# Performance work log

Hardware: AMD Instinct MI355X
Metric: run time of the kernel (lower is better)

## Reference

```python
import jax, jax.numpy as jnp
import numpy as np

HS = 1024
IMS = 4096
NHEAD = 16
EPS = 1e-5


def _layer_norm(x, g, b):
    mu = jnp.mean(x, axis=-1, keepdims=True)
    var = jnp.mean(jnp.square(x - mu), axis=-1, keepdims=True)
    return (x - mu) * jax.lax.rsqrt(var + EPS) * g + b


def setup_inputs() -> dict:
    key = jax.random.key(0)
    ks = jax.random.split(key, 10)
    B, S = 16, 512
    x = jax.random.normal(ks[0], (B, S, HS), dtype=jnp.float32)
    input_mask = jnp.zeros((B, S), dtype=jnp.float32)  # additive mask, 0 = attend
    sc = 0.02
    return {
        "x": x,
        "input_mask": input_mask,
        "qkv_w": jax.random.normal(ks[1], (3 * HS, HS), jnp.float32) * sc,
        "qkv_b": jnp.zeros((3 * HS,), jnp.float32),
        "attn_ow": jax.random.normal(ks[2], (HS, HS), jnp.float32) * sc,
        "attn_ob": jnp.zeros((HS,), jnp.float32),
        "ln1_g": jnp.ones((HS,), jnp.float32),
        "ln1_b": jnp.zeros((HS,), jnp.float32),
        "inter_w": jax.random.normal(ks[3], (IMS, HS), jnp.float32) * sc,
        "inter_b": jnp.zeros((IMS,), jnp.float32),
        "out_w": jax.random.normal(ks[4], (HS, IMS), jnp.float32) * sc,
        "out_b": jnp.zeros((HS,), jnp.float32),
        "ln2_g": jnp.ones((HS,), jnp.float32),
        "ln2_b": jnp.zeros((HS,), jnp.float32),
    }


def reference(x, input_mask, qkv_w, qkv_b, attn_ow, attn_ob, ln1_g, ln1_b,
              inter_w, inter_b, out_w, out_b, ln2_g, ln2_b):
    B, S, H = x.shape
    d = H // NHEAD
    # ---- self-attention block (pre_layer_norm=True, eval mode => no dropout) ----
    resid = x
    y = _layer_norm(x, ln1_g, ln1_b)
    qkv = jnp.einsum('bsh,eh->bse', y, qkv_w) + qkv_b  # [B,S,3H]
    q, k, v = jnp.split(qkv, 3, axis=-1)
    q = q.reshape(B, S, NHEAD, d)
    k = k.reshape(B, S, NHEAD, d)
    v = v.reshape(B, S, NHEAD, d)
    scores = jnp.einsum('bqnd,bknd->bnqk', q, k) / jnp.sqrt(jnp.float32(d))
    scores = scores + input_mask[:, None, None, :]  # additive padding mask
    probs = jax.nn.softmax(scores, axis=-1)
    ctx = jnp.einsum('bnqk,bknd->bqnd', probs, v).reshape(B, S, H)
    attn_out = jnp.einsum('bsh,oh->bso', ctx, attn_ow) + attn_ob
    x = resid + attn_out
    # ---- FFN block ----
    resid = x
    y = _layer_norm(x, ln2_g, ln2_b)
    h = jax.nn.relu(jnp.einsum('bsh,ih->bsi', y, inter_w) + inter_b)
    ffn_out = jnp.einsum('bsi,oi->bso', h, out_w) + out_b
    return resid + ffn_out
```

## Files before the change

kernel.cpp:

```cpp
#include <hip/hip_runtime.h>


using f32x4  = __attribute__((ext_vector_type(4))) float;
using f32x16 = __attribute__((ext_vector_type(16))) float;
using s16x8  = __attribute__((ext_vector_type(8))) short;
using i32x4  = __attribute__((ext_vector_type(4))) int;

__device__ __forceinline__ unsigned short f2bf(float f) {
    unsigned x = __builtin_bit_cast(unsigned, f);
    return (unsigned short)((x + 0x7fffu + ((x >> 16) & 1u)) >> 16);
}

#define GLL16(gptr, lptr)                                                     \
    __builtin_amdgcn_global_load_lds(                                         \
        (const __attribute__((address_space(1))) void*)(gptr),                \
        (__attribute__((address_space(3))) void*)(lptr), 16, 0, 0)

__global__ __launch_bounds__(256) void wconv_kernel(
    const float* __restrict__ w0, const float* __restrict__ w1,
    const float* __restrict__ w2, const float* __restrict__ w3,
    unsigned short* __restrict__ o0, unsigned short* __restrict__ o1,
    unsigned short* __restrict__ o2, unsigned short* __restrict__ o3) {
    long idx = (long)blockIdx.x * 256 + threadIdx.x;
    const float* src;
    unsigned short* dst;
    long rel;
    if (idx < 786432L)        { src = w0; dst = o0; rel = idx; }
    else if (idx < 1048576L)  { src = w1; dst = o1; rel = idx - 786432L; }
    else if (idx < 2097152L)  { src = w2; dst = o2; rel = idx - 1048576L; }
    else                      { src = w3; dst = o3; rel = idx - 2097152L; }
    float4 v = *(const float4*)(src + rel * 4);
    ushort4 o;
    o.x = f2bf(v.x); o.y = f2bf(v.y); o.z = f2bf(v.z); o.w = f2bf(v.w);
    *(ushort4*)(dst + rel * 4) = o;
}

__global__ __launch_bounds__(256) void ln_kernel(
    const float* __restrict__ x, const float* __restrict__ gw,
    const float* __restrict__ bw, unsigned short* __restrict__ y) {
    __shared__ float rbuf[8];
    const int row = blockIdx.x;
    const int t = threadIdx.x;
    const float* xr = x + (size_t)row * 1024;
    float4 v = *(const float4*)(xr + t * 4);
    float s  = v.x + v.y + v.z + v.w;
    float ss = v.x * v.x + v.y * v.y + v.z * v.z + v.w * v.w;
#pragma unroll
    for (int sh = 1; sh < 64; sh <<= 1) {
        s  += __shfl_xor(s, sh, 64);
        ss += __shfl_xor(ss, sh, 64);
    }
    int w = t >> 6;
    if ((t & 63) == 0) { rbuf[w * 2] = s; rbuf[w * 2 + 1] = ss; }
    __syncthreads();
    s  = rbuf[0] + rbuf[2] + rbuf[4] + rbuf[6];
    ss = rbuf[1] + rbuf[3] + rbuf[5] + rbuf[7];
    float mu  = s * (1.f / 1024.f);
    float var = ss * (1.f / 1024.f) - mu * mu;
    float rs  = rsqrtf(var + 1e-5f);
    float4 gv = *(const float4*)(gw + t * 4);
    float4 bv = *(const float4*)(bw + t * 4);
    ushort4 o;
    o.x = f2bf((v.x - mu) * rs * gv.x + bv.x);
    o.y = f2bf((v.y - mu) * rs * gv.y + bv.y);
    o.z = f2bf((v.z - mu) * rs * gv.z + bv.z);
    o.w = f2bf((v.w - mu) * rs * gv.w + bv.w);
    *(ushort4*)(y + (size_t)row * 1024 + t * 4) = o;
}

template <bool RELU, bool RESID, bool OUT_BF16>
__global__ __launch_bounds__(256, 2) void gemm_bt(
    const unsigned short* __restrict__ A, const unsigned short* __restrict__ Bw,
    const float* __restrict__ bias, const float* __restrict__ resid,
    void* __restrict__ Cout, int M, int N, int K) {
    __shared__ char smem[2 * 128 * 64 * 2];
    char* As = smem;
    char* Bs = smem + 128 * 64 * 2;

    const int tid = threadIdx.x;
    const int lane = tid & 63;
    const int w = tid >> 6;
    const int wr = w >> 1, wc = w & 1;
    const int g = lane >> 4;
    const int fr = lane & 15;
    const int nwg = gridDim.x * gridDim.y;
    const int L = blockIdx.y * gridDim.x + blockIdx.x;
    const int swz = (L & 7) * (nwg >> 3) + (L >> 3);
    const int m0 = (swz / gridDim.x) * 128;
    const int n0 = (swz % gridDim.x) * 128;

    f32x4 acc[4][4] = {};

    for (int kt = 0; kt < K; kt += 64) {
#pragma unroll
        for (int c = 0; c < 4; ++c) {
            int lin = (c * 256 + tid) * 16;
            int row = lin >> 7;
            int Lb = lin ^ ((row & 7) << 4);
            int colb = Lb & 127;
            const char* ga = (const char*)A + ((size_t)(m0 + row) * K + kt) * 2 + colb;
            const char* gb = (const char*)Bw + ((size_t)(n0 + row) * K + kt) * 2 + colb;
            GLL16(ga, As + lin);
            GLL16(gb, Bs + lin);
        }
        __syncthreads();
#pragma unroll
        for (int ks = 0; ks < 2; ++ks) {
            s16x8 af[4], bf[4];
#pragma unroll
            for (int mi = 0; mi < 4; ++mi) {
                int row = wr * 64 + mi * 16 + fr;
                int off = (row << 7) + ((ks * 64 + g * 16) ^ ((row & 7) << 4));
                af[mi] = *(const s16x8*)(As + off);
            }
#pragma unroll
            for (int ni = 0; ni < 4; ++ni) {
                int row = wc * 64 + ni * 16 + fr;
                int off = (row << 7) + ((ks * 64 + g * 16) ^ ((row & 7) << 4));
                bf[ni] = *(const s16x8*)(Bs + off);
            }
#pragma unroll
            for (int mi = 0; mi < 4; ++mi)
#pragma unroll
                for (int ni = 0; ni < 4; ++ni)
                    acc[mi][ni] = __builtin_amdgcn_mfma_f32_16x16x32_bf16(
                        af[mi], bf[ni], acc[mi][ni], 0, 0, 0);
        }
        __syncthreads();
    }

    float bv[4];
#pragma unroll
    for (int ni = 0; ni < 4; ++ni) bv[ni] = bias[n0 + wc * 64 + ni * 16 + fr];
#pragma unroll
    for (int mi = 0; mi < 4; ++mi) {
#pragma unroll
        for (int r = 0; r < 4; ++r) {
            int row = m0 + wr * 64 + mi * 16 + g * 4 + r;
#pragma unroll
            for (int ni = 0; ni < 4; ++ni) {
                int col = n0 + wc * 64 + ni * 16 + fr;
                float v = acc[mi][ni][r] + bv[ni];
                if (RELU) v = v > 0.f ? v : 0.f;
                if (RESID) v += resid[(size_t)row * N + col];
                if (OUT_BF16)
                    ((unsigned short*)Cout)[(size_t)row * N + col] = f2bf(v);
                else
                    ((float*)Cout)[(size_t)row * N + col] = v;
            }
        }
    }
}

template <bool RELU, bool OUT_BF16>
__global__ __launch_bounds__(512, 2) void gemm256(
    const unsigned short* __restrict__ A, const unsigned short* __restrict__ Bw,
    const float* __restrict__ bias, void* __restrict__ Cout,
    int M, int N, int K) {
    extern __shared__ char lds[];

    const int tid = threadIdx.x;
    const int lane = tid & 63;
    const int w = tid >> 6;
    const int wm = w >> 2, wn = w & 3;
    const int g = lane >> 4, fr = lane & 15;

    const int nwg = gridDim.x * gridDim.y;
    const int L = blockIdx.y * gridDim.x + blockIdx.x;
    const int swz = (L & 7) * (nwg >> 3) + (L >> 3);
    const int m0 = (swz / gridDim.x) * 256;
    const int n0 = (swz % gridDim.x) * 256;

    const int NT = K >> 6;

    auto stageA = [&](int t, int h) {
        char* dst = lds + (t & 1) * 32768 + h * 16384;
#pragma unroll
        for (int c2 = 0; c2 < 2; ++c2) {
            int lin = (c2 * 512 + tid) * 16;
            int row = lin >> 7;
            int colb = (lin & 127) ^ ((row & 7) << 4);
            GLL16((const char*)A + ((size_t)(m0 + h * 128 + row) * K + t * 64) * 2 + colb,
                  dst + lin);
        }
    };
    auto stageB = [&](int t, int h) {
        char* dst = lds + 65536 + (t & 1) * 32768 + h * 16384;
#pragma unroll
        for (int c2 = 0; c2 < 2; ++c2) {
            int lin = (c2 * 512 + tid) * 16;
            int row = lin >> 7;
            int colb = (lin & 127) ^ ((row & 7) << 4);
            GLL16((const char*)Bw + ((size_t)(n0 + h * 128 + row) * K + t * 64) * 2 + colb,
                  dst + lin);
        }
    };

    f32x4 acc[2][4][2][2] = {};
    s16x8 af[4][2];
    s16x8 bf[2][2];

    stageA(0, 0); stageB(0, 0); stageB(0, 1); stageA(0, 1);
    asm volatile("s_waitcnt vmcnt(4)" ::: "memory");
    __builtin_amdgcn_s_barrier();

    for (int t = 0; t < NT; ++t) {
        char* Ab = lds + (t & 1) * 32768;
        char* Bb = lds + 65536 + (t & 1) * 32768;
        const bool more = (t + 1 < NT);
#pragma unroll
        for (int p = 0; p < 4; ++p) {
            const int ha = p >> 1, hb = p & 1;
            if (more) {
                if (p == 0)      stageA(t + 1, 0);
                else if (p == 1) stageB(t + 1, 0);
                else if (p == 2) stageB(t + 1, 1);
                else             stageA(t + 1, 1);
            }
            if ((p & 1) == 0) {
#pragma unroll
                for (int mi2 = 0; mi2 < 4; ++mi2) {
                    int row = ha * 128 + wm * 64 + mi2 * 16 + fr;
#pragma unroll
                    for (int ks = 0; ks < 2; ++ks)
                        af[mi2][ks] = *(const s16x8*)(Ab + (row << 7) +
                                       ((ks * 64 + g * 16) ^ ((row & 7) << 4)));
                }
            }
#pragma unroll
            for (int ni2 = 0; ni2 < 2; ++ni2) {
                int row = hb * 128 + wn * 32 + ni2 * 16 + fr;
#pragma unroll
                for (int ks = 0; ks < 2; ++ks)
                    bf[ni2][ks] = *(const s16x8*)(Bb + (row << 7) +
                                   ((ks * 64 + g * 16) ^ ((row & 7) << 4)));
            }
            asm volatile("s_waitcnt vmcnt(4)" ::: "memory");
            __builtin_amdgcn_s_barrier();
            asm volatile("s_waitcnt lgkmcnt(0)" ::: "memory");
            __builtin_amdgcn_sched_barrier(0);
            __builtin_amdgcn_s_setprio(1);
#pragma unroll
            for (int mi2 = 0; mi2 < 4; ++mi2)
#pragma unroll
                for (int ni2 = 0; ni2 < 2; ++ni2)
#pragma unroll
                    for (int ks = 0; ks < 2; ++ks)
                        acc[ha][mi2][hb][ni2] = __builtin_amdgcn_mfma_f32_16x16x32_bf16(
                            af[mi2][ks], bf[ni2][ks], acc[ha][mi2][hb][ni2], 0, 0, 0);
            __builtin_amdgcn_s_setprio(0);
            __builtin_amdgcn_s_barrier();
        }
    }

#pragma unroll
    for (int ha = 0; ha < 2; ++ha)
#pragma unroll
        for (int mi2 = 0; mi2 < 4; ++mi2)
#pragma unroll
            for (int r = 0; r < 4; ++r) {
                int row = m0 + ha * 128 + wm * 64 + mi2 * 16 + g * 4 + r;
#pragma unroll
                for (int hb = 0; hb < 2; ++hb)
#pragma unroll
                    for (int ni2 = 0; ni2 < 2; ++ni2) {
                        int col = n0 + hb * 128 + wn * 32 + ni2 * 16 + fr;
                        float v = acc[ha][mi2][hb][ni2][r] + bias[col];
                        if (RELU) v = v > 0.f ? v : 0.f;
                        if (OUT_BF16)
                            ((unsigned short*)Cout)[(size_t)row * N + col] = f2bf(v);
                        else
                            ((float*)Cout)[(size_t)row * N + col] = v;
                    }
            }
}

__global__ __launch_bounds__(512, 2) void attn_kernel(
    const unsigned short* __restrict__ qkv, const float* __restrict__ mask,
    unsigned short* __restrict__ ctx) {
    extern __shared__ char smem[];

    const int tid = threadIdx.x;
    const int lane = tid & 63;
    const int w = tid >> 6;
    const int l31 = lane & 31;
    const int hi = lane >> 5;
    const int bh = blockIdx.x >> 1;
    const int b = bh >> 4, h = bh & 15;
    const int qt = (blockIdx.x & 1) * 256 + w * 32;

    const size_t rstr = 3072;
    const unsigned short* qbase = qkv + (size_t)b * 512 * rstr + h * 64;
    const unsigned short* kbase = qbase + 1024;
    const unsigned short* vbase = qbase + 2048;
    const float* mrow = mask + b * 512;

    s16x8 qf[4];
#pragma unroll
    for (int kc = 0; kc < 4; ++kc)
        qf[kc] = *(const s16x8*)(qbase + (size_t)(qt + l31) * rstr + kc * 16 + hi * 8);

    f32x16 O0 = {}, O1 = {};
    float m = -3e38f, l = 0.f;
    const int bpbase = 36 * hi * 4;

    auto stage = [&](int kt, int bufsel) {
        char* Kb = smem + bufsel * 16384;
        char* Vb = smem + 32768 + bufsel * 16384;
#pragma unroll
        for (int c = 0; c < 2; ++c) {
            int lin = (c * 512 + tid) * 16;
            int row = lin >> 7;
            int colb = (lin & 127) ^ ((row & 7) << 4);
            GLL16((const char*)kbase + (size_t)(kt * 128 + row) * rstr * 2 + colb,
                  Kb + lin);
        }
        int s = tid & 127, dg = tid >> 7;
        const unsigned short* vsrc = vbase + (size_t)(kt * 128 + s) * rstr + dg * 16;
        union { i32x4 v; unsigned short u[8]; } v0, v1;
        v0.v = *(const i32x4*)vsrc;
        v1.v = *(const i32x4*)(vsrc + 8);
#pragma unroll
        for (int j = 0; j < 8; ++j) {
            int d = dg * 16 + j;
            *(unsigned short*)(Vb + d * 256 + ((s * 2) ^ ((d & 15) << 4))) = v0.u[j];
        }
#pragma unroll
        for (int j = 0; j < 8; ++j) {
            int d = dg * 16 + 8 + j;
            *(unsigned short*)(Vb + d * 256 + ((s * 2) ^ ((d & 15) << 4))) = v1.u[j];
        }
    };

    const float C   = 0.18033688f;
    const float L2E = 1.44269504f;

    stage(0, 0);
    __syncthreads();

    for (int kt = 0; kt < 4; ++kt) {
        const int cur = kt & 1;
        if (kt < 3) stage(kt + 1, cur ^ 1);
        char* Kb = smem + cur * 16384;
        char* Vb = smem + 32768 + cur * 16384;
        const int swzk = (l31 & 7) << 4;

        f32x16 sc[4];
#pragma unroll
        for (int t = 0; t < 4; ++t) {
            f32x16 a = {};
#pragma unroll
            for (int kc = 0; kc < 4; ++kc) {
                s16x8 kf = *(const s16x8*)(Kb + (32 * t + l31) * 128 +
                                           ((kc * 32 + hi * 16) ^ swzk));
                a = __builtin_amdgcn_mfma_f32_32x32x16_bf16(kf, qf[kc], a, 0, 0, 0);
            }
            sc[t] = a;
        }

        float tm = -3e38f;
#pragma unroll
        for (int t = 0; t < 4; ++t) {
#pragma unroll
            for (int k2 = 0; k2 < 4; ++k2) {
                f32x4 mk = *(const f32x4*)(mrow + kt * 128 + 32 * t + 8 * k2 + 4 * hi);
#pragma unroll
                for (int i = 0; i < 4; ++i) {
                    float v = sc[t][4 * k2 + i] * C + mk[i] * L2E;
                    sc[t][4 * k2 + i] = v;
                    tm = fmaxf(tm, v);
                }
            }
        }
        tm = fmaxf(tm, __shfl_xor(tm, 32, 64));

        if (__any(tm > m + 11.0f)) {
            float mn = fmaxf(m, tm);
            float fac = exp2f(m - mn);
            m = mn;
            l *= fac;
            int fi = __float_as_int(fac);
#pragma unroll
            for (int r = 0; r < 16; ++r) {
                int q2 = (r & 3) + 8 * (r >> 2);
                float fq = __int_as_float(
                    __builtin_amdgcn_ds_bpermute(bpbase + q2 * 4, fi));
                O0[r] *= fq;
                O1[r] *= fq;
            }
        }

        float ts = 0.f;
#pragma unroll
        for (int t = 0; t < 4; ++t)
#pragma unroll
            for (int r = 0; r < 16; ++r) {
                float p = exp2f(sc[t][r] - m);
                sc[t][r] = p;
                ts += p;
            }
        ts += __shfl_xor(ts, 32, 64);
        l += ts;

        unsigned pk01[4][4], pk23[4][4];
#pragma unroll
        for (int t = 0; t < 4; ++t)
#pragma unroll
            for (int k = 0; k < 4; ++k) {
                unsigned r0, r1;
                asm("v_cvt_pk_bf16_f32 %0, %1, %2"
                    : "=v"(r0) : "v"(sc[t][4 * k]), "v"(sc[t][4 * k + 1]));
                asm("v_cvt_pk_bf16_f32 %0, %1, %2"
                    : "=v"(r1) : "v"(sc[t][4 * k + 2]), "v"(sc[t][4 * k + 3]));
                pk01[t][k] = r0;
                pk23[t][k] = r1;
            }

#pragma unroll
        for (int t = 0; t < 4; ++t)
#pragma unroll
            for (int cc = 0; cc < 2; ++cc) {
                unsigned a0 = pk01[t][2 * cc], b0 = pk01[t][2 * cc + 1];
                unsigned c0 = pk23[t][2 * cc], d0 = pk23[t][2 * cc + 1];
                asm("v_permlane32_swap_b32 %0, %1" : "+v"(a0), "+v"(b0));
                asm("v_permlane32_swap_b32 %0, %1" : "+v"(c0), "+v"(d0));
                union { unsigned u[4]; s16x8 v; } pf;
                pf.u[0] = a0;
                pf.u[1] = c0;
                pf.u[2] = b0;
                pf.u[3] = d0;
                const int kc = 2 * t + cc;
                {
                    int row = l31;
                    s16x8 vf = *(const s16x8*)(Vb + row * 256 +
                               ((kc * 32 + hi * 16) ^ ((row & 15) << 4)));
                    O0 = __builtin_amdgcn_mfma_f32_32x32x16_bf16(pf.v, vf, O0, 0, 0, 0);
                }
                {
                    int row = 32 + l31;
                    s16x8 vf = *(const s16x8*)(Vb + row * 256 +
                               ((kc * 32 + hi * 16) ^ ((row & 15) << 4)));
                    O1 = __builtin_amdgcn_mfma_f32_32x32x16_bf16(pf.v, vf, O1, 0, 0, 0);
                }
            }
        __syncthreads();
    }

    const int li = __float_as_int(l);
#pragma unroll
    for (int r = 0; r < 16; ++r) {
        int q2 = (r & 3) + 8 * (r >> 2);
        float lq = __int_as_float(__builtin_amdgcn_ds_bpermute(bpbase + q2 * 4, li));
        float inv = 1.f / lq;
        size_t rowg = (size_t)(b * 512 + qt + q2 + 4 * hi) * 1024 + h * 64;
        ctx[rowg + l31]      = f2bf(O0[r] * inv);
        ctx[rowg + 32 + l31] = f2bf(O1[r] * inv);
    }
}

extern "C" void kernel_launch(void* const* d_in, const int* in_sizes, int n_in,
                              void* d_out, int out_size, void* d_ws, size_t ws_size,
                              hipStream_t stream) {
    const float* x    = (const float*)d_in[0];
    const float* mask = (const float*)d_in[1];
    const float* qkvw = (const float*)d_in[2];
    const float* qkvb = (const float*)d_in[3];
    const float* ow   = (const float*)d_in[4];
    const float* ob   = (const float*)d_in[5];
    const float* ln1g = (const float*)d_in[6];
    const float* ln1b = (const float*)d_in[7];
    const float* iw   = (const float*)d_in[8];
    const float* ib   = (const float*)d_in[9];
    const float* o2w  = (const float*)d_in[10];
    const float* o2b  = (const float*)d_in[11];
    const float* ln2g = (const float*)d_in[12];
    const float* ln2b = (const float*)d_in[13];

    char* ws = (char*)d_ws;
    unsigned short* qkvbuf = (unsigned short*)(ws);
    unsigned short* ybuf   = (unsigned short*)(ws + 50331648);
    unsigned short* cbuf   = (unsigned short*)(ws + 67108864);
    float*          x2     = (float*)(ws + 83886080);
    unsigned short* wq     = (unsigned short*)(ws + 117440512);
    unsigned short* wo     = (unsigned short*)(ws + 123731968);
    unsigned short* wi     = (unsigned short*)(ws + 125829120);
    unsigned short* wo2    = (unsigned short*)(ws + 134217728);
    unsigned short* hbuf   = (unsigned short*)(ws);

    hipFuncSetAttribute(reinterpret_cast<const void*>(attn_kernel),
                        hipFuncAttributeMaxDynamicSharedMemorySize, 65536);
    hipFuncSetAttribute(reinterpret_cast<const void*>(&gemm256<false, true>),
                        hipFuncAttributeMaxDynamicSharedMemorySize, 131072);
    hipFuncSetAttribute(reinterpret_cast<const void*>(&gemm256<true, true>),
                        hipFuncAttributeMaxDynamicSharedMemorySize, 131072);

    wconv_kernel<<<12288, 256, 0, stream>>>(qkvw, ow, iw, o2w, wq, wo, wi, wo2);
    ln_kernel<<<8192, 256, 0, stream>>>(x, ln1g, ln1b, ybuf);
    gemm256<false, true><<<dim3(12, 32), 512, 131072, stream>>>(
        ybuf, wq, qkvb, qkvbuf, 8192, 3072, 1024);
    attn_kernel<<<512, 512, 65536, stream>>>(qkvbuf, mask, cbuf);
    gemm_bt<false, true, false><<<dim3(8, 64), 256, 0, stream>>>(
        cbuf, wo, ob, x, x2, 8192, 1024, 1024);
    ln_kernel<<<8192, 256, 0, stream>>>(x2, ln2g, ln2b, cbuf);
    gemm256<true, true><<<dim3(16, 32), 512, 131072, stream>>>(
        cbuf, wi, ib, hbuf, 8192, 4096, 1024);
    gemm_bt<false, true, false><<<dim3(8, 64), 256, 0, stream>>>(
        hbuf, wo2, o2b, x2, (float*)d_out, 8192, 1024, 4096);
}
```

Baseline: 312.4 us.

## Deepen GEMM prefetch pipeline to stage half-tiles two iterations ahead

Reorganizes the bf16 MFMA GEMM main loop so that global-to-LDS staging of quarter tiles runs further ahead, with A/B half-tiles for iteration t+2 issued while computing iteration t. Steady state and two peeled epilogue iterations now use explicit vmcnt waits that allow more loads in flight. The goal is to hide global load latency behind MFMA work and reduce stalls at barriers. In exchange it adds code size, more complex wait-count bookkeeping, and a risk of LDS buffer reuse races if the counts are wrong.

```diff
diff --git a/kernel.cpp b/kernel.cpp
--- a/kernel.cpp
+++ b/kernel.cpp
@@ -15,6 +15,8 @@
     __builtin_amdgcn_global_load_lds(                                         \
         (const __attribute__((address_space(1))) void*)(gptr),                \
         (__attribute__((address_space(3))) void*)(lptr), 16, 0, 0)
+
+#define VMC(N) asm volatile("s_waitcnt vmcnt(" #N ")" ::: "memory")
 
 __global__ __launch_bounds__(256) void wconv_kernel(
     const float* __restrict__ w0, const float* __restrict__ w1,
@@ -200,58 +202,77 @@
     s16x8 af[4][2];
     s16x8 bf[2][2];
 
-    stageA(0, 0); stageB(0, 0); stageB(0, 1); stageA(0, 1);
-    asm volatile("s_waitcnt vmcnt(4)" ::: "memory");
+    auto loadA = [&](const char* Ab, int ha) {
+#pragma unroll
+        for (int mi2 = 0; mi2 < 4; ++mi2) {
+            int row = ha * 128 + wm * 64 + mi2 * 16 + fr;
+#pragma unroll
+            for (int ks = 0; ks < 2; ++ks)
+                af[mi2][ks] = *(const s16x8*)(Ab + (row << 7) +
+                               ((ks * 64 + g * 16) ^ ((row & 7) << 4)));
+        }
+    };
+    auto loadB = [&](const char* Bb, int hb) {
+#pragma unroll
+        for (int ni2 = 0; ni2 < 2; ++ni2) {
+            int row = hb * 128 + wn * 32 + ni2 * 16 + fr;
+#pragma unroll
+            for (int ks = 0; ks < 2; ++ks)
+                bf[ni2][ks] = *(const s16x8*)(Bb + (row << 7) +
+                               ((ks * 64 + g * 16) ^ ((row & 7) << 4)));
+        }
+    };
+
+#define MFMAQ(HA, HB)                                                         \
+    __builtin_amdgcn_s_barrier();                                             \
+    asm volatile("s_waitcnt lgkmcnt(0)" ::: "memory");                        \
+    __builtin_amdgcn_sched_barrier(0);                                        \
+    __builtin_amdgcn_s_setprio(1);                                            \
+    _Pragma("unroll")                                                         \
+    for (int mi2 = 0; mi2 < 4; ++mi2)                                         \
+        _Pragma("unroll")                                                     \
+        for (int ni2 = 0; ni2 < 2; ++ni2)                                     \
+            _Pragma("unroll")                                                 \
+            for (int ks = 0; ks < 2; ++ks)                                    \
+                acc[HA][mi2][HB][ni2] =                                       \
+                    __builtin_amdgcn_mfma_f32_16x16x32_bf16(                  \
+                        af[mi2][ks], bf[ni2][ks], acc[HA][mi2][HB][ni2],      \
+                        0, 0, 0);                                             \
+    __builtin_amdgcn_s_setprio(0);                                            \
     __builtin_amdgcn_s_barrier();
 
-    for (int t = 0; t < NT; ++t) {
+    stageA(0, 0); stageB(0, 0); stageA(0, 1); stageB(0, 1);
+    stageA(1, 0); stageB(1, 0);
+    VMC(8);
+    __builtin_amdgcn_s_barrier();
+
+    for (int t = 0; t < NT - 2; ++t) {
         char* Ab = lds + (t & 1) * 32768;
         char* Bb = lds + 65536 + (t & 1) * 32768;
-        const bool more = (t + 1 < NT);
-#pragma unroll
-        for (int p = 0; p < 4; ++p) {
-            const int ha = p >> 1, hb = p & 1;
-            if (more) {
-                if (p == 0)      stageA(t + 1, 0);
-                else if (p == 1) stageB(t + 1, 0);
-                else if (p == 2) stageB(t + 1, 1);
-                else             stageA(t + 1, 1);
-            }
-            if ((p & 1) == 0) {
-#pragma unroll
-                for (int mi2 = 0; mi2 < 4; ++mi2) {
-                    int row = ha * 128 + wm * 64 + mi2 * 16 + fr;
-#pragma unroll
-                    for (int ks = 0; ks < 2; ++ks)
-                        af[mi2][ks] = *(const s16x8*)(Ab + (row << 7) +
-                                       ((ks * 64 + g * 16) ^ ((row & 7) << 4)));
-                }
-            }
-#pragma unroll
-            for (int ni2 = 0; ni2 < 2; ++ni2) {
-                int row = hb * 128 + wn * 32 + ni2 * 16 + fr;
-#pragma unroll
-                for (int ks = 0; ks < 2; ++ks)
-                    bf[ni2][ks] = *(const s16x8*)(Bb + (row << 7) +
-                                   ((ks * 64 + g * 16) ^ ((row & 7) << 4)));
-            }
-            asm volatile("s_waitcnt vmcnt(4)" ::: "memory");
-            __builtin_amdgcn_s_barrier();
-            asm volatile("s_waitcnt lgkmcnt(0)" ::: "memory");
-            __builtin_amdgcn_sched_barrier(0);
-            __builtin_amdgcn_s_setprio(1);
-#pragma unroll
-            for (int mi2 = 0; mi2 < 4; ++mi2)
-#pragma unroll
-                for (int ni2 = 0; ni2 < 2; ++ni2)
-#pragma unroll
-                    for (int ks = 0; ks < 2; ++ks)
-                        acc[ha][mi2][hb][ni2] = __builtin_amdgcn_mfma_f32_16x16x32_bf16(
-                            af[mi2][ks], bf[ni2][ks], acc[ha][mi2][hb][ni2], 0, 0, 0);
-            __builtin_amdgcn_s_setprio(0);
-            __builtin_amdgcn_s_barrier();
-        }
-    }
+        loadA(Ab, 0); loadB(Bb, 0); stageA(t + 1, 1); VMC(6); MFMAQ(0, 0);
+        loadB(Bb, 1);               stageB(t + 1, 1);         MFMAQ(0, 1);
+        loadA(Ab, 1); loadB(Bb, 0); stageA(t + 2, 0);         MFMAQ(1, 0);
+        loadB(Bb, 1);               stageB(t + 2, 0); VMC(8); MFMAQ(1, 1);
+    }
+    {
+        const int t = NT - 2;
+        char* Ab = lds + (t & 1) * 32768;
+        char* Bb = lds + 65536 + (t & 1) * 32768;
+        loadA(Ab, 0); loadB(Bb, 0); stageA(t + 1, 1); VMC(6); MFMAQ(0, 0);
+        loadB(Bb, 1);               stageB(t + 1, 1);         MFMAQ(0, 1);
+        loadA(Ab, 1); loadB(Bb, 0);                           MFMAQ(1, 0);
+        loadB(Bb, 1);                                 VMC(4); MFMAQ(1, 1);
+    }
+    {
+        const int t = NT - 1;
+        char* Ab = lds + (t & 1) * 32768;
+        char* Bb = lds + 65536 + (t & 1) * 32768;
+        loadA(Ab, 0); loadB(Bb, 0);                   VMC(0); MFMAQ(0, 0);
+        loadB(Bb, 1);                                         MFMAQ(0, 1);
+        loadA(Ab, 1); loadB(Bb, 0);                           MFMAQ(1, 0);
+        loadB(Bb, 1);                                         MFMAQ(1, 1);
+    }
+#undef MFMAQ
 
 #pragma unroll
     for (int ha = 0; ha < 2; ++ha)
```

After: 307.8 us. No clear change (-1.5%).
